# Optimization experiments

Measured on AMD Instinct MI355X. Metric: run time of the kernel, lower is better.

Reference implementation:

```python
import jax, jax.numpy as jnp
import numpy as np

DIM = 768
NUM_HEADS = 12
LATENT_LEN = 32


def setup_inputs() -> dict:
    key = jax.random.key(0)
    k1, k2, k3, k4 = jax.random.split(key, 4)
    x = jax.random.normal(k1, (32, 4096, DIM), dtype=jnp.float32)
    latent = jax.random.normal(k2, (1, LATENT_LEN, DIM), dtype=jnp.float32) * 0.02
    # torch nn.Linear(dim, dim): weight [out, in], bias [out]
    bound = 1.0 / np.sqrt(DIM)
    v_w = jax.random.uniform(k3, (DIM, DIM), dtype=jnp.float32, minval=-bound, maxval=bound)
    v_b = jax.random.uniform(k4, (DIM,), dtype=jnp.float32, minval=-bound, maxval=bound)
    return {"x": x, "latent": latent, "v_w": v_w, "v_b": v_b}


def reference(x, latent, v_w, v_b):
    B, N, C = x.shape
    H = NUM_HEADS
    hd = C // H
    L = LATENT_LEN
    chunk = C // L
    scale = hd ** (-0.5)

    # q: [L, H, hd] from latent (shared across batch)
    q = latent[0].reshape(L, H, hd)
    # k: [B, N, H, hd]
    k = x.reshape(B, N, H, hd)
    # attn logits: [B, H, L, N]
    attn = jnp.einsum("lhd,bnhd->bhln", q * scale, k)
    attn = jax.nn.softmax(attn, axis=-1)
    attn = attn.mean(axis=1)  # [B, L, N] (head-mean before value matmul)

    # v: Linear then split channels by latent_len -> [B, L, N, chunk]
    v = (jnp.einsum("bnc,dc->bnd", x, v_w) + v_b).reshape(B, N, L, chunk)
    out = jnp.einsum("bln,blnc->blc", attn, v.transpose(0, 2, 1, 3))
    return out.reshape(B, 1, C)
```

## Files before the change

kernel.cpp:

```cpp
#include <hip/hip_runtime.h>
#include <cstdint>


typedef short bf16x8 __attribute__((ext_vector_type(8)));
typedef float f32x4 __attribute__((ext_vector_type(4)));

#define MFMA16(a, b, c) __builtin_amdgcn_mfma_f32_16x16x32_bf16((a), (b), (c), 0, 0, 0)

__device__ __forceinline__ uint32_t pk_bf16(float a, float b) {
    return __builtin_amdgcn_perm(__float_as_uint(b), __float_as_uint(a), 0x07060302u);
}
__device__ __forceinline__ unsigned short bf16_trunc(float f) {
    return (unsigned short)(__float_as_uint(f) >> 16);
}
__device__ __forceinline__ float bf16_lo(uint32_t u) { return __uint_as_float(u << 16); }
__device__ __forceinline__ float bf16_hi(uint32_t u) { return __uint_as_float(u & 0xffff0000u); }

__global__ __launch_bounds__(256)
void k0_qconv(const float* __restrict__ latent, unsigned short* __restrict__ qbf)
{
    int i = blockIdx.x * 256 + threadIdx.x;
    int l = i / 768;
    int r = i - l * 768;
    int h = r >> 6, d = r & 63;
    qbf[(h * 32 + l) * 64 + d] = bf16_trunc(latent[i] * 0.125f);
}

__global__ __launch_bounds__(256)
void k1_logits(const float* __restrict__ x, const unsigned short* __restrict__ qbf,
               unsigned short* __restrict__ E, unsigned short* __restrict__ xT)
{
    const int b   = blockIdx.x >> 6;
    const int n0  = (blockIdx.x & 63) << 6;
    const int tid = threadIdx.x;
    const int wv  = tid >> 6;
    const int lane = tid & 63;
    const int quad = lane >> 4;
    const int lc   = lane & 15;

    __shared__ unsigned short x_lds[64][72];

    const int n = n0 + wv * 16 + lc;
    const int td = lane;

    for (int h = 0; h < 12; ++h) {
        __syncthreads();
        for (int i = tid; i < 1024; i += 256) {
            int nn = i >> 4, f4 = i & 15;
            float4 xv = *(const float4*)&x[(size_t)(b * 4096 + n0 + nn) * 768 + h * 64 + f4 * 4];
            uint2 p;
            p.x = pk_bf16(xv.x, xv.y);
            p.y = pk_bf16(xv.z, xv.w);
            *(uint2*)&x_lds[nn][f4 * 4] = p;
        }
        __syncthreads();

        const unsigned short* qh = qbf + h * 2048;
        bf16x8 a00 = *(const bf16x8*)&qh[lc * 64 + quad * 8];
        bf16x8 a01 = *(const bf16x8*)&qh[lc * 64 + 32 + quad * 8];
        bf16x8 a10 = *(const bf16x8*)&qh[(16 + lc) * 64 + quad * 8];
        bf16x8 a11 = *(const bf16x8*)&qh[(16 + lc) * 64 + 32 + quad * 8];
        bf16x8 b0  = *(const bf16x8*)&x_lds[wv * 16 + lc][quad * 8];
        bf16x8 b1  = *(const bf16x8*)&x_lds[wv * 16 + lc][32 + quad * 8];

        f32x4 c0 = {0.f, 0.f, 0.f, 0.f};
        f32x4 c1 = {0.f, 0.f, 0.f, 0.f};
        c0 = MFMA16(a00, b0, c0);
        c0 = MFMA16(a01, b1, c0);
        c1 = MFMA16(a10, b0, c1);
        c1 = MFMA16(a11, b1, c1);

        unsigned short* Eh = E + (size_t)((b * 12 + h) * 32) * 4096;
        #pragma unroll
        for (int r = 0; r < 4; ++r) {
            Eh[(quad * 4 + r) * 4096 + n]      = bf16_trunc(__expf(c0[r]));
            Eh[(16 + quad * 4 + r) * 4096 + n] = bf16_trunc(__expf(c1[r]));
        }

        unsigned short* xTrow = xT + ((size_t)b * 768 + h * 64 + td) * 4096 + n0;
        #pragma unroll
        for (int half = 0; half < 2; ++half) {
            const int nc = wv + half * 4;
            unsigned short r0 = x_lds[nc * 8 + 0][td], r1 = x_lds[nc * 8 + 1][td];
            unsigned short r2 = x_lds[nc * 8 + 2][td], r3 = x_lds[nc * 8 + 3][td];
            unsigned short r4 = x_lds[nc * 8 + 4][td], r5 = x_lds[nc * 8 + 5][td];
            unsigned short r6 = x_lds[nc * 8 + 6][td], r7 = x_lds[nc * 8 + 7][td];
            uint4 w;
            w.x = (uint32_t)r0 | ((uint32_t)r1 << 16);
            w.y = (uint32_t)r2 | ((uint32_t)r3 << 16);
            w.z = (uint32_t)r4 | ((uint32_t)r5 << 16);
            w.w = (uint32_t)r6 | ((uint32_t)r7 << 16);
            *(uint4*)&xTrow[nc * 8] = w;
        }
    }
}

__global__ __launch_bounds__(256)
void kw_weights(const unsigned short* __restrict__ E, unsigned short* __restrict__ W)
{
    const int b = blockIdx.x >> 5;
    const int l = blockIdx.x & 31;
    const int tid = threadIdx.x;
    const int wv = tid >> 6, lane = tid & 63;

    const unsigned short* Eb = E + (size_t)(b * 384 + l) * 4096;
    __shared__ float red[12][4];
    __shared__ float rsl[12];

    float s[12];
    #pragma unroll
    for (int h = 0; h < 12; ++h) {
        const uint4* p = (const uint4*)(Eb + (size_t)h * 131072 + tid * 16);
        uint4 u0 = p[0], u1 = p[1];
        float v = 0.f;
        v += bf16_lo(u0.x) + bf16_hi(u0.x) + bf16_lo(u0.y) + bf16_hi(u0.y);
        v += bf16_lo(u0.z) + bf16_hi(u0.z) + bf16_lo(u0.w) + bf16_hi(u0.w);
        v += bf16_lo(u1.x) + bf16_hi(u1.x) + bf16_lo(u1.y) + bf16_hi(u1.y);
        v += bf16_lo(u1.z) + bf16_hi(u1.z) + bf16_lo(u1.w) + bf16_hi(u1.w);
        #pragma unroll
        for (int m = 1; m < 64; m <<= 1) v += __shfl_xor(v, m);
        s[h] = v;
    }
    if (lane == 0) {
        #pragma unroll
        for (int h = 0; h < 12; ++h) red[h][wv] = s[h];
    }
    __syncthreads();
    if (tid < 12) rsl[tid] = 1.0f / (12.0f * (red[tid][0] + red[tid][1] + red[tid][2] + red[tid][3]));
    __syncthreads();

    float acc[16];
    #pragma unroll
    for (int i = 0; i < 16; ++i) acc[i] = 0.f;
    #pragma unroll
    for (int h = 0; h < 12; ++h) {
        float r = rsl[h];
        const uint4* p = (const uint4*)(Eb + (size_t)h * 131072 + tid * 16);
        uint4 u0 = p[0], u1 = p[1];
        acc[0] += bf16_lo(u0.x) * r;  acc[1] += bf16_hi(u0.x) * r;
        acc[2] += bf16_lo(u0.y) * r;  acc[3] += bf16_hi(u0.y) * r;
        acc[4] += bf16_lo(u0.z) * r;  acc[5] += bf16_hi(u0.z) * r;
        acc[6] += bf16_lo(u0.w) * r;  acc[7] += bf16_hi(u0.w) * r;
        acc[8] += bf16_lo(u1.x) * r;  acc[9] += bf16_hi(u1.x) * r;
        acc[10] += bf16_lo(u1.y) * r; acc[11] += bf16_hi(u1.y) * r;
        acc[12] += bf16_lo(u1.z) * r; acc[13] += bf16_hi(u1.z) * r;
        acc[14] += bf16_lo(u1.w) * r; acc[15] += bf16_hi(u1.w) * r;
    }
    uint4 o0, o1;
    o0.x = pk_bf16(acc[0], acc[1]);   o0.y = pk_bf16(acc[2], acc[3]);
    o0.z = pk_bf16(acc[4], acc[5]);   o0.w = pk_bf16(acc[6], acc[7]);
    o1.x = pk_bf16(acc[8], acc[9]);   o1.y = pk_bf16(acc[10], acc[11]);
    o1.z = pk_bf16(acc[12], acc[13]); o1.w = pk_bf16(acc[14], acc[15]);
    uint4* wp = (uint4*)(W + (size_t)(b * 32 + l) * 4096 + tid * 16);
    wp[0] = o0; wp[1] = o1;
}

__global__ __launch_bounds__(64)
void yacc_kernel(const unsigned short* __restrict__ xT, const unsigned short* __restrict__ W,
                 float* __restrict__ yws)
{
    const int bx  = blockIdx.x;
    const int b   = bx / 96;
    const int rem = bx - b * 96;
    const int ct  = rem % 12;
    const int g   = rem / 12;
    const int lane = threadIdx.x;
    const int quad = lane >> 4;
    const int lc   = lane & 15;
    const int c0   = ct * 64;
    const int nb   = g * 512;

    const unsigned short* xTb = xT + (size_t)b * 768 * 4096;
    const unsigned short* Wb  = W + (size_t)b * 32 * 4096;

    f32x4 acc[2][4];
    #pragma unroll
    for (int t = 0; t < 2; ++t)
        #pragma unroll
        for (int s = 0; s < 4; ++s) acc[t][s] = (f32x4){0.f, 0.f, 0.f, 0.f};

    for (int kk = 0; kk < 512; kk += 32) {
        const int n = nb + kk + quad * 8;
        bf16x8 a0 = *(const bf16x8*)&Wb[lc * 4096 + n];
        bf16x8 a1 = *(const bf16x8*)&Wb[(16 + lc) * 4096 + n];
        #pragma unroll
        for (int s = 0; s < 4; ++s) {
            bf16x8 bb = *(const bf16x8*)&xTb[(size_t)(c0 + s * 16 + lc) * 4096 + n];
            acc[0][s] = MFMA16(a0, bb, acc[0][s]);
            acc[1][s] = MFMA16(a1, bb, acc[1][s]);
        }
    }

    float* yp = yws + (size_t)((g * 32 + b) * 32) * 768;
    #pragma unroll
    for (int t = 0; t < 2; ++t)
        #pragma unroll
        for (int s = 0; s < 4; ++s)
            #pragma unroll
            for (int r = 0; r < 4; ++r)
                yp[(t * 16 + quad * 4 + r) * 768 + c0 + s * 16 + lc] = acc[t][s][r];
}

__global__ __launch_bounds__(256)
void out_kernel(const float* __restrict__ yws, const float* __restrict__ vw,
                const float* __restrict__ vb, float* __restrict__ out)
{
    const int b = blockIdx.x >> 5;
    const int l = blockIdx.x & 31;
    const int tid = threadIdx.x;
    __shared__ float y_lds[768];
    for (int c = tid; c < 768; c += 256) {
        float v = 0.f;
        #pragma unroll
        for (int g = 0; g < 8; ++g)
            v += yws[(size_t)((g * 32 + b) * 32 + l) * 768 + c];
        y_lds[c] = v;
    }
    __syncthreads();
    const int wv = tid >> 6, lane = tid & 63;
    for (int i = wv; i < 24; i += 4) {
        const int row = l * 24 + i;
        const float* wr = vw + row * 768;
        float p = 0.f;
        #pragma unroll
        for (int j = 0; j < 12; ++j)
            p += y_lds[j * 64 + lane] * wr[j * 64 + lane];
        #pragma unroll
        for (int m = 1; m < 64; m <<= 1) p += __shfl_xor(p, m);
        if (lane == 0) out[b * 768 + row] = p + vb[row];
    }
}

extern "C" void kernel_launch(void* const* d_in, const int* in_sizes, int n_in,
                              void* d_out, int out_size, void* d_ws, size_t ws_size,
                              hipStream_t stream)
{
    const float* x      = (const float*)d_in[0];
    const float* latent = (const float*)d_in[1];
    const float* vw     = (const float*)d_in[2];
    const float* vb     = (const float*)d_in[3];
    float* out = (float*)d_out;

    char* ws = (char*)d_ws;
    unsigned short* E   = (unsigned short*)ws;
    unsigned short* W   = (unsigned short*)(ws + 100663296);
    float*          yws = (float*)(ws + 109051904);
    unsigned short* xT  = (unsigned short*)(ws + 134217728);
    unsigned short* qbf = (unsigned short*)(ws + 335544320);

    k0_qconv<<<dim3(96), dim3(256), 0, stream>>>(latent, qbf);
    k1_logits<<<dim3(2048), dim3(256), 0, stream>>>(x, qbf, E, xT);
    kw_weights<<<dim3(1024), dim3(256), 0, stream>>>(E, W);
    yacc_kernel<<<dim3(3072), dim3(64), 0, stream>>>(xT, W, yws);
    out_kernel<<<dim3(1024), dim3(256), 0, stream>>>(yws, vw, vb, out);
}
```

Before: 780.2 us.

## Fuse softmax denominators into logits kernel via atomics and split heads across blocks

The logits kernel is now split so each block handles 4 heads for one 64-token tile, growing the grid threefold. The x slab is loaded once into a larger shared buffer instead of reloading per head with barriers. It also reduces the exp row sums in registers and shared memory and adds them atomically into a global sums buffer that the init kernel zeroes. The weights kernel then reads these sums instead of re-reading E a second time, removing one full pass over the exponent buffer at the cost of atomics and more shared memory per block. Some leftover unused index variables remain.

New measurement: 763.7 us. -2.1%, faster.

```diff
diff --git a/kernel.cpp b/kernel.cpp
--- a/kernel.cpp
+++ b/kernel.cpp
@@ -17,9 +17,11 @@
 __device__ __forceinline__ float bf16_hi(uint32_t u) { return __uint_as_float(u & 0xffff0000u); }
 
 __global__ __launch_bounds__(256)
-void k0_qconv(const float* __restrict__ latent, unsigned short* __restrict__ qbf)
+void k0_init(const float* __restrict__ latent, unsigned short* __restrict__ qbf,
+             float* __restrict__ sums)
 {
     int i = blockIdx.x * 256 + threadIdx.x;
+    if (i < 12288) sums[i] = 0.f;
     int l = i / 768;
     int r = i - l * 768;
     int h = r >> 6, d = r & 63;
@@ -28,40 +30,58 @@
 
 __global__ __launch_bounds__(256)
 void k1_logits(const float* __restrict__ x, const unsigned short* __restrict__ qbf,
-               unsigned short* __restrict__ E, unsigned short* __restrict__ xT)
-{
-    const int b   = blockIdx.x >> 6;
-    const int n0  = (blockIdx.x & 63) << 6;
-    const int tid = threadIdx.x;
-    const int wv  = tid >> 6;
+               unsigned short* __restrict__ E, unsigned short* __restrict__ xT,
+               float* __restrict__ sums)
+{
+    const int bx  = blockIdx.x;
+    const int b   = bx >> 7;
+    const int r7  = bx & 127;
+    const int n0  = (r7 >> 1 >> 0) << 6;
+    (void)n0;
+    const int b2   = bx / 192;
+    const int rem  = bx - b2 * 192;
+    const int nt   = rem >> 2;
+    (void)b2; (void)nt;
+    const int ntile = bx & 63;
+    const int bh    = bx >> 6;
+    const int hb    = bh % 3;
+    const int bb    = bh / 3;
+    const int nn0   = ntile << 6;
+
+    const int tid  = threadIdx.x;
+    const int wv   = tid >> 6;
     const int lane = tid & 63;
     const int quad = lane >> 4;
     const int lc   = lane & 15;
 
-    __shared__ unsigned short x_lds[64][72];
-
-    const int n = n0 + wv * 16 + lc;
+    __shared__ __align__(16) unsigned short x_lds[4][64][72];
+    __shared__ float bsum[4][32][4];
+
+    for (int i = tid; i < 4096; i += 256) {
+        const int nn = i >> 6;
+        const int j  = i & 63;
+        const int h  = j >> 4, f4 = j & 15;
+        float4 xv = *(const float4*)&x[(size_t)(bb * 4096 + nn0 + nn) * 768 + hb * 256 + j * 4];
+        uint2 p;
+        p.x = pk_bf16(xv.x, xv.y);
+        p.y = pk_bf16(xv.z, xv.w);
+        *(uint2*)&x_lds[h][nn][f4 * 4] = p;
+    }
+    __syncthreads();
+
+    const int n  = nn0 + wv * 16 + lc;
     const int td = lane;
 
-    for (int h = 0; h < 12; ++h) {
-        __syncthreads();
-        for (int i = tid; i < 1024; i += 256) {
-            int nn = i >> 4, f4 = i & 15;
-            float4 xv = *(const float4*)&x[(size_t)(b * 4096 + n0 + nn) * 768 + h * 64 + f4 * 4];
-            uint2 p;
-            p.x = pk_bf16(xv.x, xv.y);
-            p.y = pk_bf16(xv.z, xv.w);
-            *(uint2*)&x_lds[nn][f4 * 4] = p;
-        }
-        __syncthreads();
-
-        const unsigned short* qh = qbf + h * 2048;
+    #pragma unroll
+    for (int h = 0; h < 4; ++h) {
+        const int hg = hb * 4 + h;
+        const unsigned short* qh = qbf + hg * 2048;
         bf16x8 a00 = *(const bf16x8*)&qh[lc * 64 + quad * 8];
         bf16x8 a01 = *(const bf16x8*)&qh[lc * 64 + 32 + quad * 8];
         bf16x8 a10 = *(const bf16x8*)&qh[(16 + lc) * 64 + quad * 8];
         bf16x8 a11 = *(const bf16x8*)&qh[(16 + lc) * 64 + 32 + quad * 8];
-        bf16x8 b0  = *(const bf16x8*)&x_lds[wv * 16 + lc][quad * 8];
-        bf16x8 b1  = *(const bf16x8*)&x_lds[wv * 16 + lc][32 + quad * 8];
+        bf16x8 b0  = *(const bf16x8*)&x_lds[h][wv * 16 + lc][quad * 8];
+        bf16x8 b1  = *(const bf16x8*)&x_lds[h][wv * 16 + lc][32 + quad * 8];
 
         f32x4 c0 = {0.f, 0.f, 0.f, 0.f};
         f32x4 c1 = {0.f, 0.f, 0.f, 0.f};
@@ -70,21 +90,38 @@
         c1 = MFMA16(a10, b0, c1);
         c1 = MFMA16(a11, b1, c1);
 
-        unsigned short* Eh = E + (size_t)((b * 12 + h) * 32) * 4096;
+        unsigned short* Eh = E + (size_t)((bb * 12 + hg) * 32) * 4096;
+        float sv[8];
         #pragma unroll
         for (int r = 0; r < 4; ++r) {
-            Eh[(quad * 4 + r) * 4096 + n]      = bf16_trunc(__expf(c0[r]));
-            Eh[(16 + quad * 4 + r) * 4096 + n] = bf16_trunc(__expf(c1[r]));
-        }
-
-        unsigned short* xTrow = xT + ((size_t)b * 768 + h * 64 + td) * 4096 + n0;
+            uint32_t u0 = __float_as_uint(__expf(c0[r]));
+            uint32_t u1 = __float_as_uint(__expf(c1[r]));
+            Eh[(quad * 4 + r) * 4096 + n]      = (unsigned short)(u0 >> 16);
+            Eh[(16 + quad * 4 + r) * 4096 + n] = (unsigned short)(u1 >> 16);
+            sv[r]     = __uint_as_float(u0 & 0xffff0000u);
+            sv[4 + r] = __uint_as_float(u1 & 0xffff0000u);
+        }
+        #pragma unroll
+        for (int m = 1; m < 16; m <<= 1) {
+            #pragma unroll
+            for (int k = 0; k < 8; ++k) sv[k] += __shfl_xor(sv[k], m);
+        }
+        if (lc == 0) {
+            #pragma unroll
+            for (int r = 0; r < 4; ++r) {
+                bsum[h][quad * 4 + r][wv]      = sv[r];
+                bsum[h][16 + quad * 4 + r][wv] = sv[4 + r];
+            }
+        }
+
+        unsigned short* xTrow = xT + ((size_t)bb * 768 + hg * 64 + td) * 4096 + nn0;
         #pragma unroll
         for (int half = 0; half < 2; ++half) {
             const int nc = wv + half * 4;
-            unsigned short r0 = x_lds[nc * 8 + 0][td], r1 = x_lds[nc * 8 + 1][td];
-            unsigned short r2 = x_lds[nc * 8 + 2][td], r3 = x_lds[nc * 8 + 3][td];
-            unsigned short r4 = x_lds[nc * 8 + 4][td], r5 = x_lds[nc * 8 + 5][td];
-            unsigned short r6 = x_lds[nc * 8 + 6][td], r7 = x_lds[nc * 8 + 7][td];
+            unsigned short r0 = x_lds[h][nc * 8 + 0][td], r1 = x_lds[h][nc * 8 + 1][td];
+            unsigned short r2 = x_lds[h][nc * 8 + 2][td], r3 = x_lds[h][nc * 8 + 3][td];
+            unsigned short r4 = x_lds[h][nc * 8 + 4][td], r5 = x_lds[h][nc * 8 + 5][td];
+            unsigned short r6 = x_lds[h][nc * 8 + 6][td], r7 = x_lds[h][nc * 8 + 7][td];
             uint4 w;
             w.x = (uint32_t)r0 | ((uint32_t)r1 << 16);
             w.y = (uint32_t)r2 | ((uint32_t)r3 << 16);
@@ -93,40 +130,26 @@
             *(uint4*)&xTrow[nc * 8] = w;
         }
     }
-}
-
-__global__ __launch_bounds__(256)
-void kw_weights(const unsigned short* __restrict__ E, unsigned short* __restrict__ W)
+
+    __syncthreads();
+    if (tid < 128) {
+        const int h = tid >> 5, l = tid & 31;
+        atomicAdd(&sums[(bb * 12 + hb * 4 + h) * 32 + l],
+                  bsum[h][l][0] + bsum[h][l][1] + bsum[h][l][2] + bsum[h][l][3]);
+    }
+}
+
+__global__ __launch_bounds__(256)
+void kw_weights(const unsigned short* __restrict__ E, const float* __restrict__ sums,
+                unsigned short* __restrict__ W)
 {
     const int b = blockIdx.x >> 5;
     const int l = blockIdx.x & 31;
     const int tid = threadIdx.x;
-    const int wv = tid >> 6, lane = tid & 63;
 
     const unsigned short* Eb = E + (size_t)(b * 384 + l) * 4096;
-    __shared__ float red[12][4];
     __shared__ float rsl[12];
-
-    float s[12];
-    #pragma unroll
-    for (int h = 0; h < 12; ++h) {
-        const uint4* p = (const uint4*)(Eb + (size_t)h * 131072 + tid * 16);
-        uint4 u0 = p[0], u1 = p[1];
-        float v = 0.f;
-        v += bf16_lo(u0.x) + bf16_hi(u0.x) + bf16_lo(u0.y) + bf16_hi(u0.y);
-        v += bf16_lo(u0.z) + bf16_hi(u0.z) + bf16_lo(u0.w) + bf16_hi(u0.w);
-        v += bf16_lo(u1.x) + bf16_hi(u1.x) + bf16_lo(u1.y) + bf16_hi(u1.y);
-        v += bf16_lo(u1.z) + bf16_hi(u1.z) + bf16_lo(u1.w) + bf16_hi(u1.w);
-        #pragma unroll
-        for (int m = 1; m < 64; m <<= 1) v += __shfl_xor(v, m);
-        s[h] = v;
-    }
-    if (lane == 0) {
-        #pragma unroll
-        for (int h = 0; h < 12; ++h) red[h][wv] = s[h];
-    }
-    __syncthreads();
-    if (tid < 12) rsl[tid] = 1.0f / (12.0f * (red[tid][0] + red[tid][1] + red[tid][2] + red[tid][3]));
+    if (tid < 12) rsl[tid] = 1.0f / (12.0f * sums[(b * 12 + tid) * 32 + l]);
     __syncthreads();
 
     float acc[16];
@@ -242,15 +265,16 @@
     float* out = (float*)d_out;
 
     char* ws = (char*)d_ws;
-    unsigned short* E   = (unsigned short*)ws;
-    unsigned short* W   = (unsigned short*)(ws + 100663296);
-    float*          yws = (float*)(ws + 109051904);
-    unsigned short* xT  = (unsigned short*)(ws + 134217728);
-    unsigned short* qbf = (unsigned short*)(ws + 335544320);
-
-    k0_qconv<<<dim3(96), dim3(256), 0, stream>>>(latent, qbf);
-    k1_logits<<<dim3(2048), dim3(256), 0, stream>>>(x, qbf, E, xT);
-    kw_weights<<<dim3(1024), dim3(256), 0, stream>>>(E, W);
+    unsigned short* E    = (unsigned short*)ws;
+    unsigned short* W    = (unsigned short*)(ws + 100663296);
+    float*          yws  = (float*)(ws + 109051904);
+    unsigned short* xT   = (unsigned short*)(ws + 134217728);
+    unsigned short* qbf  = (unsigned short*)(ws + 335544320);
+    float*          sums = (float*)(ws + 335609856);
+
+    k0_init<<<dim3(96), dim3(256), 0, stream>>>(latent, qbf, sums);
+    k1_logits<<<dim3(6144), dim3(256), 0, stream>>>(x, qbf, E, xT, sums);
+    kw_weights<<<dim3(1024), dim3(256), 0, stream>>>(E, sums, W);
     yacc_kernel<<<dim3(3072), dim3(64), 0, stream>>>(xT, W, yws);
     out_kernel<<<dim3(1024), dim3(256), 0, stream>>>(yws, vw, vb, out);
 }
```
